# Kernel optimization log

Measured on AMD Instinct MI355X. Metric: run time of the kernel, lower is better.

The kernel has to match this reference:

```python
import jax, jax.numpy as jnp
import numpy as np

M = 0.25      # margin m
GAMMA = 64.0  # scale gamma
N, D = 8192, 128
NUM_CLASSES = 512


def setup_inputs() -> dict:
    key = jax.random.key(0)
    k1, k2 = jax.random.split(key)
    inputs = jax.random.normal(k1, (N, D), dtype=jnp.float32)
    targets = jax.random.randint(k2, (N,), 0, NUM_CLASSES, dtype=jnp.int64)
    return {"inputs": inputs, "targets": targets}


def reference(inputs, targets):
    # L2-normalize rows -> cosine similarity matrix [n, n]
    x = inputs / jnp.linalg.norm(inputs, axis=1, keepdims=True)
    sim = x @ x.T
    # positive mask: same label (includes diagonal, matching the torch code)
    mask = targets[:, None] == targets[None, :]

    Op, On = 1.0 + M, -M
    delta_p, delta_n = 1.0 - M, M

    sim_d = jax.lax.stop_gradient(sim)  # .detach() in torch
    ap = jnp.maximum(Op - sim_d, 0.0)
    an = jnp.maximum(sim_d + On, 0.0)

    logit_p = -ap * (sim - delta_p) * GAMMA
    logit_n = an * (sim - delta_n) * GAMMA

    neg_inf = jnp.float32(-jnp.inf)
    # per-row logsumexp over positives of -logit_p, over negatives of logit_n
    lp = jax.nn.logsumexp(jnp.where(mask, -logit_p, neg_inf), axis=1)
    ln = jax.nn.logsumexp(jnp.where(mask, neg_inf, logit_n), axis=1)

    return jnp.mean(jax.nn.softplus(ln + lp))
```

## Files before the change

### kernel.cpp

```cpp
#include <hip/hip_runtime.h>
#include <math.h>


#define NR    8192
#define DIMK  128
#define NT    64
#define NBLKS 512
#define MAXC  64

#define CE1 9.6089795f
#define CE0 -2.4022449f

typedef __attribute__((ext_vector_type(8))) short short8;
typedef __attribute__((ext_vector_type(4))) float f32x4;
typedef __attribute__((address_space(3))) uint32_t lds_u32;
typedef const __attribute__((address_space(1))) uint32_t glb_u32;

__device__ __forceinline__ unsigned short bf16_rne(float f) {
  uint32_t u = __float_as_uint(f);
  u += 0x7FFFu + ((u >> 16) & 1u);
  return (unsigned short)(u >> 16);
}

__device__ __forceinline__ float fexp2(float x) {
#if __has_builtin(__builtin_amdgcn_exp2f)
  return __builtin_amdgcn_exp2f(x);
#else
  return exp2f(x);
#endif
}


__global__ __launch_bounds__(256) void normalize_split_kernel(
    const float* __restrict__ x, unsigned short* __restrict__ xhi,
    unsigned short* __restrict__ xlo, float* __restrict__ gP,
    float* __restrict__ gN, int* __restrict__ counter) {
  if (blockIdx.x < 32)      gP[blockIdx.x * 256 + threadIdx.x] = 0.f;
  else if (blockIdx.x < 64) gN[(blockIdx.x - 32) * 256 + threadIdx.x] = 0.f;
  if (blockIdx.x == 64 && threadIdx.x == 0) *counter = 0;

  const int wave = threadIdx.x >> 6;
  const int lane = threadIdx.x & 63;
  const int row  = blockIdx.x * 4 + wave;
  const float2 v = ((const float2*)(x + (size_t)row * DIMK))[lane];
  float ss = v.x * v.x + v.y * v.y;
  #pragma unroll
  for (int s = 1; s < 64; s <<= 1) ss += __shfl_xor(ss, s);
  const float r = rsqrtf(ss);
  const float a = v.x * r, b = v.y * r;
  const unsigned short ha = bf16_rne(a), hb = bf16_rne(b);
  const float haf = __uint_as_float((uint32_t)ha << 16);
  const float hbf = __uint_as_float((uint32_t)hb << 16);
  ushort2 hi, lo;
  hi.x = ha; hi.y = hb;
  lo.x = bf16_rne(a - haf); lo.y = bf16_rne(b - hbf);
  ((ushort2*)xhi)[(size_t)row * 64 + lane] = hi;
  ((ushort2*)xlo)[(size_t)row * 64 + lane] = lo;
}

__global__ __launch_bounds__(512, 2) void simloss_kernel(
    const unsigned short* __restrict__ xhi, const unsigned short* __restrict__ xlo,
    const int* __restrict__ tgt, float* __restrict__ gP, float* __restrict__ gN,
    int* __restrict__ counter, float* __restrict__ out) {
  __shared__ unsigned short S[32768];
  __shared__ float colbuf[2][4][128];
  __shared__ float red[512];
  __shared__ int midx[MAXC];
  __shared__ int scnt;
  __shared__ int islast;

  const int tid  = threadIdx.x;
  const int wave = tid >> 6, lane = tid & 63;
  const int wy = wave & 3, wx = wave >> 2;
  const int q = lane >> 4, mcol = lane & 15;
  const bool isStage = (wy == 1) || (wy == 2);
  const bool isFlush = (wy == 0);
  const int srank = (wy - 1) + wx * 2;

  {
    if (tid == 0) scnt = 0;
    __syncthreads();
    const int4* t4 = (const int4*)tgt;
    const int me = (int)blockIdx.x;
    for (int v = tid; v < NR / 4; v += 512) {
      const int4 tv = t4[v];
      const int base = v * 4;
      if (tv.x == me) { const int s_ = atomicAdd(&scnt, 1); if (s_ < MAXC) midx[s_] = base; }
      if (tv.y == me) { const int s_ = atomicAdd(&scnt, 1); if (s_ < MAXC) midx[s_] = base + 1; }
      if (tv.z == me) { const int s_ = atomicAdd(&scnt, 1); if (s_ < MAXC) midx[s_] = base + 2; }
      if (tv.w == me) { const int s_ = atomicAdd(&scnt, 1); if (s_ < MAXC) midx[s_] = base + 3; }
    }
    __syncthreads();
    const int m = (scnt < MAXC) ? scnt : MAXC;
    float* Sf = (float*)S;
    for (int v = tid; v < m * 32; v += 512) {
      const int r = v >> 5, c4 = v & 31;
      const int row = midx[r];
      const ushort4 h = ((const ushort4*)(xhi + (size_t)row * DIMK))[c4];
      const ushort4 l = ((const ushort4*)(xlo + (size_t)row * DIMK))[c4];
      float* d = &Sf[r * 129 + c4 * 4];
      d[0] = __uint_as_float((uint32_t)h.x << 16) + __uint_as_float((uint32_t)l.x << 16);
      d[1] = __uint_as_float((uint32_t)h.y << 16) + __uint_as_float((uint32_t)l.y << 16);
      d[2] = __uint_as_float((uint32_t)h.z << 16) + __uint_as_float((uint32_t)l.z << 16);
      d[3] = __uint_as_float((uint32_t)h.w << 16) + __uint_as_float((uint32_t)l.w << 16);
    }
    __syncthreads();
    for (int pr = tid; pr < m * m; pr += 512) {
      const int i = pr / m, j = pr - i * m;
      const float* vi = &Sf[i * 129];
      const float* vj = &Sf[j * 129];
      float s = 0.f;
      #pragma unroll 8
      for (int d = 0; d < 128; ++d) s = fmaf(vi[d], vj[d], s);
      const int gi = midx[i];
      const float ep = __expf(fmaxf(1.25f - s, 0.f) * fmaf(s, 64.f, -48.f));
      atomicAdd(&gP[gi], ep);
      if (i != j) {
        const float u = fmaxf(fmaf(s, CE1, CE0), 0.f);
        atomicAdd(&gN[gi], -fexp2(u * u));
      }
    }
    __syncthreads();
  }

  const int p  = blockIdx.x >> 4;
  const int b  = blockIdx.x & 15;
  const int n1 = NT - p;
  const int t0 = (b * (NT + 1)) >> 4;
  const int t1 = ((b + 1) * (NT + 1)) >> 4;
  const int ntile = t1 - t0;
  const int p2 = NT - 1 - p;

  int cur_bi = (t0 < n1) ? p : p2;

  auto stageA = [&](int bi) {
    const unsigned short* gh = xhi + (size_t)bi * 128 * DIMK;
    const unsigned short* gl = xlo + (size_t)bi * 128 * DIMK;
    #pragma unroll
    for (int g = 0; g < 4; ++g) {
      const int r  = wave * 16 + g * 4 + (lane >> 4);
      const int sc = (lane & 15) ^ (r & 15);
      __builtin_amdgcn_global_load_lds((glb_u32*)(gh + (size_t)r * DIMK + sc * 8),
          (lds_u32*)&S[(wave * 16 + g * 4) * 128], 16, 0, 0);
      __builtin_amdgcn_global_load_lds((glb_u32*)(gl + (size_t)r * DIMK + sc * 8),
          (lds_u32*)&S[16384 + (wave * 16 + g * 4) * 128], 16, 0, 0);
    }
  };
  auto stageB = [&](int bj, int buf) {
    const unsigned short* gb = xhi + (size_t)bj * 128 * DIMK;
    unsigned short* dst = &S[buf * 16384];
    #pragma unroll
    for (int g = 0; g < 8; ++g) {
      const int r  = srank * 32 + g * 4 + (lane >> 4);
      const int sc = (lane & 15) ^ (r & 15);
      __builtin_amdgcn_global_load_lds((glb_u32*)(gb + (size_t)r * DIMK + sc * 8),
          (lds_u32*)&dst[(srank * 32 + g * 4) * 128], 16, 0, 0);
    }
  };

  short8 Ah[2][4], Al[2][4];
  auto extractA = [&]() {
    #pragma unroll
    for (int fr = 0; fr < 2; ++fr) {
      const int r = wy * 32 + fr * 16 + mcol;
      #pragma unroll
      for (int ks = 0; ks < 4; ++ks) {
        const int pc = (ks * 4 + q) ^ mcol;
        Ah[fr][ks] = *(const short8*)&S[r * 128 + pc * 8];
        Al[fr][ks] = *(const short8*)&S[16384 + r * 128 + pc * 8];
      }
    }
  };

  float rowN[2][4] = {{0.f}};
  auto flushRows = [&](int bi_) {
    #pragma unroll
    for (int fr = 0; fr < 2; ++fr)
      #pragma unroll
      for (int rg = 0; rg < 4; ++rg) {
        float vn = rowN[fr][rg];
        #pragma unroll
        for (int m2 = 1; m2 < 16; m2 <<= 1) vn += __shfl_xor(vn, m2);
        if (mcol == 0)
          atomicAdd(&gN[bi_ * 128 + wy * 32 + fr * 16 + q * 4 + rg], vn);
      }
  };

  stageA(cur_bi);
  __syncthreads();
  extractA();
  __builtin_amdgcn_s_waitcnt(49279);
  __builtin_amdgcn_s_barrier();
  if (isStage) stageB((t0 < n1) ? p + t0 : p2 + (t0 - n1), 0);

  for (int tl = 0; tl < ntile; ++tl) {
    const int ix = t0 + tl;
    const int bi = (ix < n1) ? p : p2;
    const int bj = (ix < n1) ? p + ix : p2 + (ix - n1);

    if (bi != cur_bi) {
      flushRows(cur_bi);
      cur_bi = bi;
      stageA(cur_bi);
      __syncthreads();
      extractA();
      #pragma unroll
      for (int fr = 0; fr < 2; ++fr)
        #pragma unroll
        for (int rg = 0; rg < 4; ++rg) rowN[fr][rg] = 0.f;
      __builtin_amdgcn_s_waitcnt(49279);
      __builtin_amdgcn_s_barrier();
      if (isStage) stageB(bj, tl & 1);
    }

    if (isStage) __builtin_amdgcn_s_waitcnt(112);
    __builtin_amdgcn_s_barrier();

    if (tl + 1 < ntile) {
      const int ix2 = ix + 1;
      if ((ix2 < n1) == (ix < n1)) {
        const int bj2 = (ix2 < n1) ? p + ix2 : p2 + (ix2 - n1);
        if (isStage) stageB(bj2, (tl + 1) & 1);
      }
    }

    const unsigned short* Bb = &S[(tl & 1) * 16384];
    f32x4 acc[2][4];
    #pragma unroll
    for (int fr = 0; fr < 2; ++fr)
      #pragma unroll
      for (int fc = 0; fc < 4; ++fc)
        acc[fr][fc] = (f32x4){0.f, 0.f, 0.f, 0.f};
    #pragma unroll
    for (int ks = 0; ks < 4; ++ks) {
      short8 bh[4];
      #pragma unroll
      for (int fc = 0; fc < 4; ++fc) {
        const int rb = wx * 64 + fc * 16 + mcol;
        const int pc = (ks * 4 + q) ^ mcol;
        bh[fc] = *(const short8*)&Bb[rb * 128 + pc * 8];
      }
      #pragma unroll
      for (int fc = 0; fc < 4; ++fc) {
        acc[0][fc] = __builtin_amdgcn_mfma_f32_16x16x32_bf16(Ah[0][ks], bh[fc], acc[0][fc], 0, 0, 0);
        acc[1][fc] = __builtin_amdgcn_mfma_f32_16x16x32_bf16(Ah[1][ks], bh[fc], acc[1][fc], 0, 0, 0);
        acc[0][fc] = __builtin_amdgcn_mfma_f32_16x16x32_bf16(Al[0][ks], bh[fc], acc[0][fc], 0, 0, 0);
        acc[1][fc] = __builtin_amdgcn_mfma_f32_16x16x32_bf16(Al[1][ks], bh[fc], acc[1][fc], 0, 0, 0);
      }
    }

    float cN[4] = {0.f, 0.f, 0.f, 0.f};
#define EPILOGUE(DIAG_)                                                      \
    {                                                                        \
      _Pragma("unroll")                                                      \
      for (int fr = 0; fr < 2; ++fr) {                                       \
        _Pragma("unroll")                                                    \
        for (int rg = 0; rg < 4; ++rg) {                                     \
          float vn = 0.f;                                                    \
          _Pragma("unroll")                                                  \
          for (int fc = 0; fc < 4; ++fc) {                                   \
            const float s = acc[fr][fc][rg];                                 \
            const float u = fmaxf(fmaf(s, CE1, CE0), 0.f);                   \
            float e = fexp2(u * u);                                          \
            if (DIAG_) {                                                     \
              const int rl = wy * 32 + fr * 16 + q * 4 + rg;                 \
              const int cl = wx * 64 + fc * 16 + mcol;                       \
              e = (rl == cl) ? 0.f : e;                                      \
            }                                                                \
            vn += e;                                                         \
            cN[fc] += e;                                                     \
          }                                                                  \
          rowN[fr][rg] += vn;                                                \
        }                                                                    \
      }                                                                      \
    }
    if (bj == bi) EPILOGUE(true) else EPILOGUE(false)
#undef EPILOGUE

    #pragma unroll
    for (int fc = 0; fc < 4; ++fc) {
      cN[fc] += __shfl_xor(cN[fc], 16);
      cN[fc] += __shfl_xor(cN[fc], 32);
    }
    if (q == 0) {
      #pragma unroll
      for (int fc = 0; fc < 4; ++fc)
        colbuf[tl & 1][wy][wx * 64 + fc * 16 + mcol] = cN[fc];
    }
    __builtin_amdgcn_s_waitcnt(49279);
    __builtin_amdgcn_s_barrier();

    if (isFlush && bj != bi) {
      const int col = wx * 64 + lane;
      float sn = 0.f;
      #pragma unroll
      for (int w = 0; w < 4; ++w) sn += colbuf[tl & 1][w][col];
      atomicAdd(&gN[bj * 128 + col], sn);
    }
  }
  flushRows(cur_bi);

  __builtin_amdgcn_s_waitcnt(0);
  __syncthreads();
  if (tid == 0) islast = (atomicAdd(counter, 1) == NBLKS - 1) ? 1 : 0;
  __syncthreads();
  if (islast) {
    float local = 0.f;
    #pragma unroll 1
    for (int bb = 0; bb < 2; ++bb) {
      const int base = bb * 4096 + tid * 8;
      float pv[8], nv[8];
      #pragma unroll
      for (int u = 0; u < 8; ++u) pv[u] = atomicAdd(&gP[base + u], 0.0f);
      #pragma unroll
      for (int u = 0; u < 8; ++u) nv[u] = atomicAdd(&gN[base + u], 0.0f);
      #pragma unroll
      for (int u = 0; u < 8; ++u) local += log1pf(pv[u] * nv[u]);
    }
    red[tid] = local;
    __syncthreads();
    for (int s2 = 256; s2 > 0; s2 >>= 1) {
      if (tid < s2) red[tid] += red[tid + s2];
      __syncthreads();
    }
    if (tid == 0) out[0] = red[0] / (float)NR;
  }
}

extern "C" void kernel_launch(void* const* d_in, const int* in_sizes, int n_in,
                              void* d_out, int out_size, void* d_ws, size_t ws_size,
                              hipStream_t stream) {
  const float* x  = (const float*)d_in[0];
  const int* tgt  = (const int*)d_in[1];
  float* out      = (float*)d_out;

  unsigned short* xhi = (unsigned short*)d_ws;
  unsigned short* xlo = xhi + (size_t)NR * DIMK;
  float* gP = (float*)((char*)d_ws + (size_t)NR * DIMK * 4);
  float* gN = gP + NR;
  int* counter = (int*)(gN + NR);

  normalize_split_kernel<<<NR / 4, 256, 0, stream>>>(x, xhi, xlo, gP, gN, counter);
  simloss_kernel<<<NBLKS, 512, 0, stream>>>(xhi, xlo, tgt, gP, gN, counter, out);
}
```

Measured before the change: 121.7 us.

## Move per-class positive correction into separate finalize kernel

Moves the per-class positive-pair computation (target scan, gathering same-label rows, m×m dot products) out of the main similarity kernel into a new finalize kernel launched after it. The finalize kernel accumulates positives and negative corrections in shared memory instead of global atomics, then does a per-class log1p reduction with a last-block final sum. This is meant to remove the prologue and its serialization from the heavy GEMM kernel and to drop the gP buffer and its global atomics, at the cost of an extra kernel launch and a second read of the target array. MAXC is also raised to 96.

```diff
diff --git a/kernel.cpp b/kernel.cpp
--- a/kernel.cpp
+++ b/kernel.cpp
@@ -6,7 +6,8 @@
 #define DIMK  128
 #define NT    64
 #define NBLKS 512
-#define MAXC  64
+#define NCLS  512
+#define MAXC  96
 
 #define CE1 9.6089795f
 #define CE0 -2.4022449f
@@ -33,11 +34,10 @@
 
 __global__ __launch_bounds__(256) void normalize_split_kernel(
     const float* __restrict__ x, unsigned short* __restrict__ xhi,
-    unsigned short* __restrict__ xlo, float* __restrict__ gP,
-    float* __restrict__ gN, int* __restrict__ counter) {
-  if (blockIdx.x < 32)      gP[blockIdx.x * 256 + threadIdx.x] = 0.f;
-  else if (blockIdx.x < 64) gN[(blockIdx.x - 32) * 256 + threadIdx.x] = 0.f;
-  if (blockIdx.x == 64 && threadIdx.x == 0) *counter = 0;
+    unsigned short* __restrict__ xlo, float* __restrict__ gN,
+    int* __restrict__ counter) {
+  if (blockIdx.x < 32) gN[blockIdx.x * 256 + threadIdx.x] = 0.f;
+  if (blockIdx.x == 32 && threadIdx.x == 0) *counter = 0;
 
   const int wave = threadIdx.x >> 6;
   const int lane = threadIdx.x & 63;
@@ -60,14 +60,9 @@
 
 __global__ __launch_bounds__(512, 2) void simloss_kernel(
     const unsigned short* __restrict__ xhi, const unsigned short* __restrict__ xlo,
-    const int* __restrict__ tgt, float* __restrict__ gP, float* __restrict__ gN,
-    int* __restrict__ counter, float* __restrict__ out) {
+    float* __restrict__ gN) {
   __shared__ unsigned short S[32768];
   __shared__ float colbuf[2][4][128];
-  __shared__ float red[512];
-  __shared__ int midx[MAXC];
-  __shared__ int scnt;
-  __shared__ int islast;
 
   const int tid  = threadIdx.x;
   const int wave = tid >> 6, lane = tid & 63;
@@ -76,52 +71,6 @@
   const bool isStage = (wy == 1) || (wy == 2);
   const bool isFlush = (wy == 0);
   const int srank = (wy - 1) + wx * 2;
-
-  {
-    if (tid == 0) scnt = 0;
-    __syncthreads();
-    const int4* t4 = (const int4*)tgt;
-    const int me = (int)blockIdx.x;
-    for (int v = tid; v < NR / 4; v += 512) {
-      const int4 tv = t4[v];
-      const int base = v * 4;
-      if (tv.x == me) { const int s_ = atomicAdd(&scnt, 1); if (s_ < MAXC) midx[s_] = base; }
-      if (tv.y == me) { const int s_ = atomicAdd(&scnt, 1); if (s_ < MAXC) midx[s_] = base + 1; }
-      if (tv.z == me) { const int s_ = atomicAdd(&scnt, 1); if (s_ < MAXC) midx[s_] = base + 2; }
-      if (tv.w == me) { const int s_ = atomicAdd(&scnt, 1); if (s_ < MAXC) midx[s_] = base + 3; }
-    }
-    __syncthreads();
-    const int m = (scnt < MAXC) ? scnt : MAXC;
-    float* Sf = (float*)S;
-    for (int v = tid; v < m * 32; v += 512) {
-      const int r = v >> 5, c4 = v & 31;
-      const int row = midx[r];
-      const ushort4 h = ((const ushort4*)(xhi + (size_t)row * DIMK))[c4];
-      const ushort4 l = ((const ushort4*)(xlo + (size_t)row * DIMK))[c4];
-      float* d = &Sf[r * 129 + c4 * 4];
-      d[0] = __uint_as_float((uint32_t)h.x << 16) + __uint_as_float((uint32_t)l.x << 16);
-      d[1] = __uint_as_float((uint32_t)h.y << 16) + __uint_as_float((uint32_t)l.y << 16);
-      d[2] = __uint_as_float((uint32_t)h.z << 16) + __uint_as_float((uint32_t)l.z << 16);
-      d[3] = __uint_as_float((uint32_t)h.w << 16) + __uint_as_float((uint32_t)l.w << 16);
-    }
-    __syncthreads();
-    for (int pr = tid; pr < m * m; pr += 512) {
-      const int i = pr / m, j = pr - i * m;
-      const float* vi = &Sf[i * 129];
-      const float* vj = &Sf[j * 129];
-      float s = 0.f;
-      #pragma unroll 8
-      for (int d = 0; d < 128; ++d) s = fmaf(vi[d], vj[d], s);
-      const int gi = midx[i];
-      const float ep = __expf(fmaxf(1.25f - s, 0.f) * fmaf(s, 64.f, -48.f));
-      atomicAdd(&gP[gi], ep);
-      if (i != j) {
-        const float u = fmaxf(fmaf(s, CE1, CE0), 0.f);
-        atomicAdd(&gN[gi], -fexp2(u * u));
-      }
-    }
-    __syncthreads();
-  }
 
   const int p  = blockIdx.x >> 4;
   const int b  = blockIdx.x & 15;
@@ -299,27 +248,95 @@
     }
   }
   flushRows(cur_bi);
+}
+
+__global__ __launch_bounds__(256) void finalize_kernel(
+    const unsigned short* __restrict__ xhi, const unsigned short* __restrict__ xlo,
+    const int* __restrict__ tgt, const float* __restrict__ gN,
+    float* __restrict__ gC, int* __restrict__ counter, float* __restrict__ out) {
+  __shared__ float Sf[MAXC * 129];
+  __shared__ float Pv[MAXC];
+  __shared__ float Ncor[MAXC];
+  __shared__ int midx[MAXC];
+  __shared__ float red[256];
+  __shared__ int scnt;
+  __shared__ int islast;
+
+  const int tid = threadIdx.x;
+  const int me  = (int)blockIdx.x;
+
+  if (tid == 0) scnt = 0;
+  if (tid < MAXC) { Pv[tid] = 0.f; Ncor[tid] = 0.f; }
+  __syncthreads();
+
+  const int4* t4 = (const int4*)tgt;
+  for (int v = tid; v < NR / 4; v += 256) {
+    const int4 tv = t4[v];
+    const int base = v * 4;
+    if (tv.x == me) { const int s_ = atomicAdd(&scnt, 1); if (s_ < MAXC) midx[s_] = base; }
+    if (tv.y == me) { const int s_ = atomicAdd(&scnt, 1); if (s_ < MAXC) midx[s_] = base + 1; }
+    if (tv.z == me) { const int s_ = atomicAdd(&scnt, 1); if (s_ < MAXC) midx[s_] = base + 2; }
+    if (tv.w == me) { const int s_ = atomicAdd(&scnt, 1); if (s_ < MAXC) midx[s_] = base + 3; }
+  }
+  __syncthreads();
+  const int m = (scnt < MAXC) ? scnt : MAXC;
+
+  for (int v = tid; v < m * 32; v += 256) {
+    const int r = v >> 5, c4 = v & 31;
+    const int row = midx[r];
+    const ushort4 h = ((const ushort4*)(xhi + (size_t)row * DIMK))[c4];
+    const ushort4 l = ((const ushort4*)(xlo + (size_t)row * DIMK))[c4];
+    float* d = &Sf[r * 129 + c4 * 4];
+    d[0] = __uint_as_float((uint32_t)h.x << 16) + __uint_as_float((uint32_t)l.x << 16);
+    d[1] = __uint_as_float((uint32_t)h.y << 16) + __uint_as_float((uint32_t)l.y << 16);
+    d[2] = __uint_as_float((uint32_t)h.z << 16) + __uint_as_float((uint32_t)l.z << 16);
+    d[3] = __uint_as_float((uint32_t)h.w << 16) + __uint_as_float((uint32_t)l.w << 16);
+  }
+  __syncthreads();
+
+  for (int pr = tid; pr < m * m; pr += 256) {
+    const int i = pr / m, j = pr - i * m;
+    const float* vi = &Sf[i * 129];
+    const float* vj = &Sf[j * 129];
+    float s = 0.f;
+    #pragma unroll 8
+    for (int d = 0; d < 128; ++d) s = fmaf(vi[d], vj[d], s);
+    const float ep = __expf(fmaxf(1.25f - s, 0.f) * fmaf(s, 64.f, -48.f));
+    atomicAdd(&Pv[i], ep);
+    if (i != j) {
+      const float u = fmaxf(fmaf(s, CE1, CE0), 0.f);
+      atomicAdd(&Ncor[i], fexp2(u * u));
+    }
+  }
+  __syncthreads();
+
+  float local = 0.f;
+  for (int r = tid; r < m; r += 256) {
+    const int gi = midx[r];
+    local += log1pf(Pv[r] * (gN[gi] - Ncor[r]));
+  }
+  red[tid] = local;
+  __syncthreads();
+  #pragma unroll
+  for (int s2 = 128; s2 > 0; s2 >>= 1) {
+    if (tid < s2) red[tid] += red[tid + s2];
+    __syncthreads();
+  }
+  if (tid == 0) atomicExch(&gC[me], red[0]);
 
   __builtin_amdgcn_s_waitcnt(0);
   __syncthreads();
-  if (tid == 0) islast = (atomicAdd(counter, 1) == NBLKS - 1) ? 1 : 0;
+  if (tid == 0) islast = (atomicAdd(counter, 1) == NCLS - 1) ? 1 : 0;
   __syncthreads();
   if (islast) {
-    float local = 0.f;
-    #pragma unroll 1
-    for (int bb = 0; bb < 2; ++bb) {
-      const int base = bb * 4096 + tid * 8;
-      float pv[8], nv[8];
-      #pragma unroll
-      for (int u = 0; u < 8; ++u) pv[u] = atomicAdd(&gP[base + u], 0.0f);
-      #pragma unroll
-      for (int u = 0; u < 8; ++u) nv[u] = atomicAdd(&gN[base + u], 0.0f);
-      #pragma unroll
-      for (int u = 0; u < 8; ++u) local += log1pf(pv[u] * nv[u]);
-    }
-    red[tid] = local;
+    float sum = 0.f;
+    #pragma unroll
+    for (int u = 0; u < 2; ++u)
+      sum += atomicAdd(&gC[tid * 2 + u], 0.0f);
+    red[tid] = sum;
     __syncthreads();
-    for (int s2 = 256; s2 > 0; s2 >>= 1) {
+    #pragma unroll
+    for (int s2 = 128; s2 > 0; s2 >>= 1) {
       if (tid < s2) red[tid] += red[tid + s2];
       __syncthreads();
     }
@@ -336,10 +353,11 @@
 
   unsigned short* xhi = (unsigned short*)d_ws;
   unsigned short* xlo = xhi + (size_t)NR * DIMK;
-  float* gP = (float*)((char*)d_ws + (size_t)NR * DIMK * 4);
-  float* gN = gP + NR;
-  int* counter = (int*)(gN + NR);
-
-  normalize_split_kernel<<<NR / 4, 256, 0, stream>>>(x, xhi, xlo, gP, gN, counter);
-  simloss_kernel<<<NBLKS, 512, 0, stream>>>(xhi, xlo, tgt, gP, gN, counter, out);
-}
+  float* gN = (float*)((char*)d_ws + (size_t)NR * DIMK * 4);
+  float* gC = gN + NR;
+  int* counter = (int*)(gC + NCLS);
+
+  normalize_split_kernel<<<NR / 4, 256, 0, stream>>>(x, xhi, xlo, gN, counter);
+  simloss_kernel<<<NBLKS, 512, 0, stream>>>(xhi, xlo, gN);
+  finalize_kernel<<<NCLS, 256, 0, stream>>>(xhi, xlo, tgt, gN, gC, counter, out);
+}
```

New measurement: 111.9 us. 1.09x faster.
